# Optimization experiments

Hardware: AMD Instinct MI355X
Metric: run time of the kernel (lower is better)

Reference implementation:

```python
import jax, jax.numpy as jnp
import numpy as np

B, T, D, H, K, M = 2, 2048, 1024, 16, 3, 16384
HD = D // H
SCALE = D * (H ** 0.5)  # faithful to source: n_embd / n_head**(-0.5)


def _normalize(v, axis=-1, eps=1e-12):
    # torch F.normalize: v / max(||v||, eps)
    n = jnp.sqrt(jnp.sum(v * v, axis=axis, keepdims=True))
    return v / jnp.maximum(n, eps)


def setup_inputs() -> dict:
    key = jax.random.key(0)
    ks = jax.random.split(key, 12)
    s = 1.0 / np.sqrt(D)
    return {
        "x": jax.random.normal(ks[0], (B, T, D), jnp.float32),
        "Wq": jax.random.normal(ks[1], (D, D), jnp.float32) * s,
        "bq": jax.random.normal(ks[2], (D,), jnp.float32) * 0.01,
        "Wk": jax.random.normal(ks[3], (D, D), jnp.float32) * s,
        "bk": jax.random.normal(ks[4], (D,), jnp.float32) * 0.01,
        "Wv": jax.random.normal(ks[5], (D, D), jnp.float32) * s,
        "bv": jax.random.normal(ks[6], (D,), jnp.float32) * 0.01,
        "Wo": jax.random.normal(ks[7], (D, D), jnp.float32) * s,
        "bo": jax.random.normal(ks[8], (D,), jnp.float32) * 0.01,
        "gate_bias": jax.random.normal(ks[9], (H, 1, 1), jnp.float32),
        "mem_bank": jax.random.normal(ks[10], (B, M, 2, D), jnp.float32) * s,
        "knn_idx": jax.random.randint(ks[11], (B, T, K), 0, M, jnp.int32),
    }


def reference(x, Wq, bq, Wk, bk, Wv, bv, Wo, bo, gate_bias, mem_bank, knn_idx):
    b, t, d = x.shape
    # projections + L2-normalize q,k (as in source)
    q = _normalize(x @ Wq.T + bq)
    k = _normalize(x @ Wk.T + bk)
    v = x @ Wv.T + bv
    # split heads: b t (h hd) -> b h t hd
    q = q.reshape(b, t, H, HD).transpose(0, 2, 1, 3)
    k = k.reshape(b, t, H, HD).transpose(0, 2, 1, 3)
    v = v.reshape(b, t, H, HD).transpose(0, 2, 1, 3)
    # local causal attention (hand-rolled, dropout is eval no-op)
    qk = jnp.einsum('bhid,bhjd->bhij', q, k) * SCALE  # [b,h,t,t]
    causal = jnp.triu(jnp.ones((t, t), dtype=bool), 1)
    qk = jnp.where(causal, -jnp.inf, qk)
    attn = jax.nn.softmax(qk, axis=-1)
    qkv = jnp.einsum('bhij,bhjd->bhid', attn, v)  # [b,h,t,hd]
    # kNN memory retrieval: gather top-k (key,value) memories per token
    mem = mem_bank[jnp.arange(b)[:, None, None], knn_idx]  # [b,t,k,2,D]
    mem_k = mem[..., 0, :].reshape(b, t, K, H, HD).transpose(0, 3, 1, 2, 4)  # [b,h,t,k,hd]
    mem_v = mem[..., 1, :].reshape(b, t, K, H, HD).transpose(0, 3, 1, 2, 4)
    mem_qk = jnp.einsum('bhtd,bhtkd->bhtk', q.astype(jnp.float32), mem_k) * SCALE
    mem_attn = jax.nn.softmax(mem_qk, axis=-1)
    mem_qkv = jnp.einsum('bhtk,bhtkd->bhtd', mem_attn, mem_v)
    # per-head gated blend, bf16 round-trip (source casts to bfloat16)
    combined = mem_qkv * gate_bias + qkv * (1.0 - gate_bias)  # gate [H,1,1] broadcasts
    combined = combined.astype(jnp.bfloat16).astype(jnp.float32)
    y = combined.transpose(0, 2, 1, 3).reshape(b, t, d)  # b h t hd -> b t D
    return y @ Wo.T + bo
```

## Files before the change

### kernel.cpp

```cpp
#include <hip/hip_runtime.h>
#include <math.h>

#define B_ 2
#define T_ 2048
#define D_ 1024
#define H_ 16
#define HD_ 64
#define M_ 16384
#define SCALE_F 4096.0f
#define LDP 3072
#define ST 72

using short8 = __attribute__((ext_vector_type(8))) short;
using bf16x8 = __attribute__((ext_vector_type(8))) __bf16;
using f32x4  = __attribute__((ext_vector_type(4))) float;

__device__ __forceinline__ unsigned short f2bf(float x){
  unsigned u = __builtin_bit_cast(unsigned, x);
  u += 0x7fffu + ((u >> 16) & 1u);
  return (unsigned short)(u >> 16);
}
__device__ __forceinline__ float bf2f(unsigned short h){
  unsigned u = ((unsigned)h) << 16;
  return __builtin_bit_cast(float, u);
}

__device__ __forceinline__ float wsum(float v){
  #pragma unroll
  for (int off = 32; off; off >>= 1) v += __shfl_xor(v, off);
  return v;
}

__device__ __forceinline__ void ld_g2l16(const unsigned short* g, unsigned short* l){
  __builtin_amdgcn_global_load_lds(
      (const __attribute__((address_space(1))) void*)g,
      (__attribute__((address_space(3))) void*)l, 16, 0, 0);
}

__global__ __launch_bounds__(256)
void cvt_all(const float* __restrict__ x, const float* __restrict__ Wq,
             const float* __restrict__ Wk, const float* __restrict__ Wv,
             const float* __restrict__ Wo,
             unsigned short* __restrict__ Xhi, unsigned short* __restrict__ Xlo,
             unsigned short* __restrict__ Whi, unsigned short* __restrict__ Wlo,
             unsigned short* __restrict__ Wohi)
{
  const int i = blockIdx.x*256 + threadIdx.x;
  const float* src; unsigned short* hi; unsigned short* lo = nullptr; int rel;
  if      (i < 1048576){ src = x;  hi = Xhi;            lo = Xlo;            rel = i; }
  else if (i < 1310720){ src = Wq; hi = Whi;            lo = Wlo;            rel = i - 1048576; }
  else if (i < 1572864){ src = Wk; hi = Whi + 1048576;  lo = Wlo + 1048576;  rel = i - 1310720; }
  else if (i < 1835008){ src = Wv; hi = Whi + 2097152;                       rel = i - 1572864; }
  else                 { src = Wo; hi = Wohi;                                rel = i - 1835008; }
  float4 v = *(const float4*)(src + (size_t)rel*4);
  unsigned short h0=f2bf(v.x), h1=f2bf(v.y), h2=f2bf(v.z), h3=f2bf(v.w);
  uint2 hh; hh.x = (unsigned)h0 | ((unsigned)h1 << 16);
            hh.y = (unsigned)h2 | ((unsigned)h3 << 16);
  *(uint2*)(hi + (size_t)rel*4) = hh;
  if (lo){
    uint2 ll;
    ll.x = (unsigned)f2bf(v.x-bf2f(h0)) | ((unsigned)f2bf(v.y-bf2f(h1)) << 16);
    ll.y = (unsigned)f2bf(v.z-bf2f(h2)) | ((unsigned)f2bf(v.w-bf2f(h3)) << 16);
    *(uint2*)(lo + (size_t)rel*4) = ll;
  }
}

template<bool COMP>
__global__ __launch_bounds__(256)
void gemm_lds(const unsigned short* __restrict__ Ahi_g, const unsigned short* __restrict__ Alo_g,
              const unsigned short* __restrict__ Bhi_g, const unsigned short* __restrict__ Blo_g,
              const float* __restrict__ bias0, const float* __restrict__ bias1,
              const float* __restrict__ bias2,
              float* __restrict__ C, int ldc)
{
  __shared__ __align__(16) unsigned short Ah[128*32];
  __shared__ __align__(16) unsigned short Bh[128*32];
  __shared__ __align__(16) unsigned short Al[COMP ? 128*32 : 8];
  __shared__ __align__(16) unsigned short Bl[COMP ? 128*32 : 8];

  const int tid = threadIdx.x, lane = tid & 63, wv = tid >> 6;
  const int wm = wv >> 1, wn = wv & 1;
  const int mi = lane & 15, quad = lane >> 4;

  int bid = blockIdx.y*gridDim.x + blockIdx.x;
  const int cpx = (gridDim.x*gridDim.y) >> 3;
  bid = (bid & 7)*cpx + (bid >> 3);
  const int n0 = (bid % gridDim.x) * 128;
  const int m0 = (bid / gridDim.x) * 128;

  const int seg = n0 >> 10;
  const float* bias = (seg == 0) ? bias0 : (seg == 1) ? bias1 : bias2;
  const int nw = n0 & 1023;
  const bool comp = COMP && (seg < 2);

  f32x4 acc[4][4];
  #pragma unroll
  for (int a = 0; a < 4; ++a)
    #pragma unroll
    for (int b = 0; b < 4; ++b)
      acc[a][b] = (f32x4){0.f, 0.f, 0.f, 0.f};

  for (int k0 = 0; k0 < 1024; k0 += 32){
    __syncthreads();
    #pragma unroll
    for (int t = 0; t < 2; ++t){
      int j = wv*128 + t*64 + lane;
      int row = j >> 2, c16 = j & 3;
      size_t ga = (size_t)(m0 + row)*1024 + k0 + c16*8;
      size_t gb = (size_t)(n0 + row)*1024 + k0 + c16*8;
      ld_g2l16(Ahi_g + ga, Ah + j*8);
      ld_g2l16(Bhi_g + gb, Bh + j*8);
      if (comp){
        ld_g2l16(Alo_g + ga, Al + j*8);
        ld_g2l16(Blo_g + gb, Bl + j*8);
      }
    }
    __syncthreads();

    bf16x8 ah[4], al[4];
    #pragma unroll
    for (int a = 0; a < 4; ++a){
      int r = wm*64 + a*16 + mi;
      ah[a] = __builtin_bit_cast(bf16x8, *(const short8*)(Ah + r*32 + quad*8));
      if (comp)
        al[a] = __builtin_bit_cast(bf16x8, *(const short8*)(Al + r*32 + quad*8));
    }
    #pragma unroll
    for (int b = 0; b < 4; ++b){
      int r = wn*64 + b*16 + mi;
      bf16x8 bh = __builtin_bit_cast(bf16x8, *(const short8*)(Bh + r*32 + quad*8));
      if (comp){
        bf16x8 bl = __builtin_bit_cast(bf16x8, *(const short8*)(Bl + r*32 + quad*8));
        #pragma unroll
        for (int a = 0; a < 4; ++a){
          acc[a][b] = __builtin_amdgcn_mfma_f32_16x16x32_bf16(al[a], bh, acc[a][b], 0, 0, 0);
          acc[a][b] = __builtin_amdgcn_mfma_f32_16x16x32_bf16(ah[a], bl, acc[a][b], 0, 0, 0);
          acc[a][b] = __builtin_amdgcn_mfma_f32_16x16x32_bf16(ah[a], bh, acc[a][b], 0, 0, 0);
        }
      } else {
        #pragma unroll
        for (int a = 0; a < 4; ++a)
          acc[a][b] = __builtin_amdgcn_mfma_f32_16x16x32_bf16(ah[a], bh, acc[a][b], 0, 0, 0);
      }
    }
  }
  #pragma unroll
  for (int a = 0; a < 4; ++a)
    #pragma unroll
    for (int b = 0; b < 4; ++b)
      #pragma unroll
      for (int r = 0; r < 4; ++r){
        int row  = m0 + wm*64 + a*16 + quad*4 + r;
        int coll = wn*64 + b*16 + mi;
        C[(size_t)row*ldc + n0 + coll] = acc[a][b][r] + bias[nw + coll];
      }
}

__global__ __launch_bounds__(256)
void norm_split(const float* __restrict__ P,
                unsigned short* __restrict__ Qhi, unsigned short* __restrict__ Qlo,
                unsigned short* __restrict__ Khi, unsigned short* __restrict__ Klo,
                unsigned short* __restrict__ Vbf)
{
  const int row = blockIdx.x, tid = threadIdx.x;
  const int bb = row >> 11, t = row & 2047;
  const int lane = tid & 63, wv = tid >> 6;
  const size_t base = (size_t)row * LDP;
  float4 q4 = *(const float4*)(P + base + tid*4);
  float4 k4 = *(const float4*)(P + base + 1024 + tid*4);
  float4 v4 = *(const float4*)(P + base + 2048 + tid*4);
  float sq = wsum(q4.x*q4.x + q4.y*q4.y + q4.z*q4.z + q4.w*q4.w);
  float sk = wsum(k4.x*k4.x + k4.y*k4.y + k4.z*k4.z + k4.w*k4.w);
  __shared__ float rq[4], rk[4];
  if (lane == 0){ rq[wv] = sq; rk[wv] = sk; }
  __syncthreads();
  float cq = 1.f / fmaxf(sqrtf(rq[0]+rq[1]+rq[2]+rq[3]), 1e-12f);
  float ck = 1.f / fmaxf(sqrtf(rk[0]+rk[1]+rk[2]+rk[3]), 1e-12f);
  float qf[4] = {q4.x*cq, q4.y*cq, q4.z*cq, q4.w*cq};
  float kf[4] = {k4.x*ck, k4.y*ck, k4.z*ck, k4.w*ck};

  const int h = tid >> 4, d0 = (tid & 15)*4;
  const size_t ob = ((size_t)(bb*H_ + h)*T_ + t)*64 + d0;

  uint2 qh, ql, kh, kl, vv;
  unsigned short t0,t1,t2,t3;
  t0=f2bf(qf[0]); t1=f2bf(qf[1]); t2=f2bf(qf[2]); t3=f2bf(qf[3]);
  qh.x = t0 | ((unsigned)t1<<16); qh.y = t2 | ((unsigned)t3<<16);
  ql.x = f2bf(qf[0]-bf2f(t0)) | ((unsigned)f2bf(qf[1]-bf2f(t1))<<16);
  ql.y = f2bf(qf[2]-bf2f(t2)) | ((unsigned)f2bf(qf[3]-bf2f(t3))<<16);
  t0=f2bf(kf[0]); t1=f2bf(kf[1]); t2=f2bf(kf[2]); t3=f2bf(kf[3]);
  kh.x = t0 | ((unsigned)t1<<16); kh.y = t2 | ((unsigned)t3<<16);
  kl.x = f2bf(kf[0]-bf2f(t0)) | ((unsigned)f2bf(kf[1]-bf2f(t1))<<16);
  kl.y = f2bf(kf[2]-bf2f(t2)) | ((unsigned)f2bf(kf[3]-bf2f(t3))<<16);
  vv.x = f2bf(v4.x) | ((unsigned)f2bf(v4.y)<<16);
  vv.y = f2bf(v4.z) | ((unsigned)f2bf(v4.w)<<16);
  *(uint2*)(Qhi + ob) = qh;  *(uint2*)(Qlo + ob) = ql;
  *(uint2*)(Khi + ob) = kh;  *(uint2*)(Klo + ob) = kl;
  *(uint2*)(Vbf + ob) = vv;
}

__device__ __forceinline__ void stage_issue(
    const unsigned short* __restrict__ Khi_g, const unsigned short* __restrict__ Klo_g,
    const unsigned short* __restrict__ Vbf, size_t hb, int jt, int tid,
    uint2* khr, uint2* klr, ushort4* vra, ushort4* vrb)
{
  #pragma unroll
  for (int i = 0; i < 4; ++i){
    int idx = tid + i*256;
    int row = idx >> 4, c4 = idx & 15;
    size_t g = (hb + jt*64 + row)*64 + c4*4;
    khr[i] = *(const uint2*)(Khi_g + g);
    klr[i] = *(const uint2*)(Klo_g + g);
  }
  #pragma unroll
  for (int i = 0; i < 2; ++i){
    int idx = tid + i*256;
    int rp = idx & 31, d4 = idx >> 5;
    size_t g = (hb + jt*64 + 2*rp)*64 + d4*4;
    vra[i] = *(const ushort4*)(Vbf + g);
    vrb[i] = *(const ushort4*)(Vbf + g + 64);
  }
}

__device__ __forceinline__ void stage_write(char* bufc, int tid,
    const uint2* khr, const uint2* klr, const ushort4* vra, const ushort4* vrb)
{
  unsigned short* Kh = (unsigned short*)bufc;
  unsigned short* Kl = (unsigned short*)(bufc + 9216);
  unsigned* vt = (unsigned*)(bufc + 18432);
  #pragma unroll
  for (int i = 0; i < 4; ++i){
    int idx = tid + i*256;
    int row = idx >> 4, c4 = idx & 15;
    *(uint2*)(Kh + row*ST + c4*4) = khr[i];
    *(uint2*)(Kl + row*ST + c4*4) = klr[i];
  }
  #pragma unroll
  for (int i = 0; i < 2; ++i){
    int idx = tid + i*256;
    int rp = idx & 31, d4 = idx >> 5;
    vt[(d4*4+0)*36 + rp] = (unsigned)vra[i].x | ((unsigned)vrb[i].x << 16);
    vt[(d4*4+1)*36 + rp] = (unsigned)vra[i].y | ((unsigned)vrb[i].y << 16);
    vt[(d4*4+2)*36 + rp] = (unsigned)vra[i].z | ((unsigned)vrb[i].z << 16);
    vt[(d4*4+3)*36 + rp] = (unsigned)vra[i].w | ((unsigned)vrb[i].w << 16);
  }
}

__device__ __forceinline__ void attn_tile(
    const unsigned short* __restrict__ Kh, const unsigned short* __restrict__ Kl,
    const unsigned short* __restrict__ Vt, unsigned short* __restrict__ pw,
    const bf16x8* qh, const bf16x8* ql,
    f32x4* O, float& mr, float& lr,
    bool last, int relrow, int mi, int quad)
{
  f32x4 st[4];
  #pragma unroll
  for (int mt = 0; mt < 4; ++mt) st[mt] = (f32x4){0.f,0.f,0.f,0.f};
  __builtin_amdgcn_s_setprio(1);
  #pragma unroll
  for (int mt = 0; mt < 4; ++mt){
    int krow = mt*16 + mi;
    #pragma unroll
    for (int ks = 0; ks < 2; ++ks){
      bf16x8 kh = __builtin_bit_cast(bf16x8, *(const short8*)(Kh + krow*ST + ks*32 + quad*8));
      bf16x8 kl = __builtin_bit_cast(bf16x8, *(const short8*)(Kl + krow*ST + ks*32 + quad*8));
      st[mt] = __builtin_amdgcn_mfma_f32_16x16x32_bf16(kl, qh[ks], st[mt], 0, 0, 0);
      st[mt] = __builtin_amdgcn_mfma_f32_16x16x32_bf16(kh, ql[ks], st[mt], 0, 0, 0);
      st[mt] = __builtin_amdgcn_mfma_f32_16x16x32_bf16(kh, qh[ks], st[mt], 0, 0, 0);
    }
  }
  __builtin_amdgcn_s_setprio(0);

  float tmax = -INFINITY;
  #pragma unroll
  for (int mt = 0; mt < 4; ++mt)
    #pragma unroll
    for (int r = 0; r < 4; ++r){
      float s = st[mt][r] * SCALE_F;
      if (last){
        int key = mt*16 + quad*4 + r;
        if (key > relrow) s = -INFINITY;
      }
      st[mt][r] = s;
      tmax = fmaxf(tmax, s);
    }
  tmax = fmaxf(tmax, __shfl_xor(tmax, 16));
  tmax = fmaxf(tmax, __shfl_xor(tmax, 32));
  float mnew = fmaxf(mr, tmax);
  float alpha = __expf(mr - mnew);
  mr = mnew;
  float tsum = 0.f;
  #pragma unroll
  for (int mt = 0; mt < 4; ++mt)
    #pragma unroll
    for (int r = 0; r < 4; ++r){
      float p = __expf(st[mt][r] - mnew);
      st[mt][r] = p;
      tsum += p;
    }
  tsum += __shfl_xor(tsum, 16);
  tsum += __shfl_xor(tsum, 32);
  lr = lr*alpha + tsum;

  #pragma unroll
  for (int mt = 0; mt < 4; ++mt){
    uint2 pk;
    pk.x = (unsigned)f2bf(st[mt][0]) | ((unsigned)f2bf(st[mt][1]) << 16);
    pk.y = (unsigned)f2bf(st[mt][2]) | ((unsigned)f2bf(st[mt][3]) << 16);
    *(uint2*)(pw + mi*ST + mt*16 + quad*4) = pk;
  }

  float af[4];
  #pragma unroll
  for (int r = 0; r < 4; ++r) af[r] = __shfl(alpha, quad*4 + r);
  #pragma unroll
  for (int dn = 0; dn < 4; ++dn)
    #pragma unroll
    for (int r = 0; r < 4; ++r) O[dn][r] *= af[r];

  __builtin_amdgcn_s_setprio(1);
  #pragma unroll
  for (int kt = 0; kt < 2; ++kt){
    bf16x8 pf = __builtin_bit_cast(bf16x8, *(const short8*)(pw + mi*ST + kt*32 + quad*8));
    #pragma unroll
    for (int dn = 0; dn < 4; ++dn){
      bf16x8 vf = __builtin_bit_cast(bf16x8, *(const short8*)(Vt + (dn*16 + mi)*ST + kt*32 + quad*8));
      O[dn] = __builtin_amdgcn_mfma_f32_16x16x32_bf16(pf, vf, O[dn], 0, 0, 0);
    }
  }
  __builtin_amdgcn_s_setprio(0);
}

__global__ __launch_bounds__(256)
void attn_knn(const unsigned short* __restrict__ Qhi, const unsigned short* __restrict__ Qlo,
              const unsigned short* __restrict__ Khi_g, const unsigned short* __restrict__ Klo_g,
              const unsigned short* __restrict__ Vbf,
              const float* __restrict__ mem_bank, const int* __restrict__ knn_idx,
              const float* __restrict__ gate_bias, unsigned short* __restrict__ comb)
{
  __shared__ __align__(16) char smpool[64512];
  float* qkvs = (float*)smpool;

  const int bb = blockIdx.z, h = blockIdx.y;
  const int p = blockIdx.x;
  const int jA = p, jB = 31 - p;
  const int tid = threadIdx.x, lane = tid & 63, wv = tid >> 6;
  const int mi = lane & 15, quad = lane >> 4;
  const int relrow = wv*16 + mi;
  const size_t hb = (size_t)(bb*H_ + h)*T_;
  unsigned short* pw = (unsigned short*)(smpool + 55296) + wv*1152;

  const int sub = lane & 3;
  const int grp = tid >> 2;
  const int base = lane & 60;
  int idxP[2];
  idxP[0] = (sub < 3) ? knn_idx[((size_t)bb*T_ + jA*64 + grp)*3 + sub] : 0;
  idxP[1] = (sub < 3) ? knn_idx[((size_t)bb*T_ + jB*64 + grp)*3 + sub] : 0;

  bf16x8 qhA[2], qlA[2], qhB[2], qlB[2];
  #pragma unroll
  for (int ks = 0; ks < 2; ++ks){
    qhA[ks] = __builtin_bit_cast(bf16x8, *(const uint4*)(Qhi + (hb + jA*64 + relrow)*64 + ks*32 + quad*8));
    qlA[ks] = __builtin_bit_cast(bf16x8, *(const uint4*)(Qlo + (hb + jA*64 + relrow)*64 + ks*32 + quad*8));
    qhB[ks] = __builtin_bit_cast(bf16x8, *(const uint4*)(Qhi + (hb + jB*64 + relrow)*64 + ks*32 + quad*8));
    qlB[ks] = __builtin_bit_cast(bf16x8, *(const uint4*)(Qlo + (hb + jB*64 + relrow)*64 + ks*32 + quad*8));
  }

  f32x4 OA[4], OB[4];
  #pragma unroll
  for (int dn = 0; dn < 4; ++dn){
    OA[dn] = (f32x4){0.f,0.f,0.f,0.f};
    OB[dn] = (f32x4){0.f,0.f,0.f,0.f};
  }
  float mA = -INFINITY, lA = 0.f, mB = -INFINITY, lB = 0.f;

  const int ntiles = jB + 1;

  uint2 khr[4], klr[4]; ushort4 vra[2], vrb[2];
  stage_issue(Khi_g, Klo_g, Vbf, hb, 0, tid, khr, klr, vra, vrb);
  stage_write(smpool, tid, khr, klr, vra, vrb);
  stage_issue(Khi_g, Klo_g, Vbf, hb, 1, tid, khr, klr, vra, vrb);

  int cur = 0;
  for (int jt = 0; jt < ntiles; ++jt){
    __syncthreads();
    if (jt + 1 < ntiles){
      stage_write(smpool + (cur^1)*27648, tid, khr, klr, vra, vrb);
      if (jt + 2 < ntiles)
        stage_issue(Khi_g, Klo_g, Vbf, hb, jt+2, tid, khr, klr, vra, vrb);
    }
    char* bufc = smpool + cur*27648;
    const unsigned short* Kh = (const unsigned short*)bufc;
    const unsigned short* Kl = (const unsigned short*)(bufc + 9216);
    const unsigned short* Vt = (const unsigned short*)(bufc + 18432);
    if (jt <= jA)
      attn_tile(Kh, Kl, Vt, pw, qhA, qlA, OA, mA, lA, jt == jA, relrow, mi, quad);
    attn_tile(Kh, Kl, Vt, pw, qhB, qlB, OB, mB, lB, jt == jB, relrow, mi, quad);
    cur ^= 1;
  }

  __syncthreads();
  {
    float liA[4], liB[4];
    #pragma unroll
    for (int r = 0; r < 4; ++r){
      liA[r] = 1.f / __shfl(lA, quad*4 + r);
      liB[r] = 1.f / __shfl(lB, quad*4 + r);
    }
    #pragma unroll
    for (int dn = 0; dn < 4; ++dn)
      #pragma unroll
      for (int r = 0; r < 4; ++r){
        qkvs[(      wv*16 + quad*4 + r)*68 + dn*16 + mi] = OA[dn][r] * liA[r];
        qkvs[(64 +  wv*16 + quad*4 + r)*68 + dn*16 + mi] = OB[dn][r] * liB[r];
      }
  }
  __syncthreads();

  const float g = gate_bias[h];
  const float gq = 1.f - g;

  #pragma unroll
  for (int it = 0; it < 2; ++it){
    const int jq = it ? jB : jA;
    const int trow = jq*64 + grp;
    const int lrow = it*64 + grp;

    int idxs[3];
    #pragma unroll
    for (int kk = 0; kk < 3; ++kk) idxs[kk] = __shfl(idxP[it], base + kk);

    float4 mk4[3][4], mv4[3][4];
    #pragma unroll
    for (int kk = 0; kk < 3; ++kk){
      const float* mk = mem_bank + (((size_t)bb*M_ + idxs[kk])*2 + 0)*D_ + h*HD_ + sub*16;
      const float* mv = mem_bank + (((size_t)bb*M_ + idxs[kk])*2 + 1)*D_ + h*HD_ + sub*16;
      #pragma unroll
      for (int j4 = 0; j4 < 4; ++j4){
        mk4[kk][j4] = *(const float4*)(mk + j4*4);
        mv4[kk][j4] = *(const float4*)(mv + j4*4);
      }
    }

    float qf[16];
    {
      const unsigned short* qp = Qhi + (hb + trow)*64 + sub*16;
      const unsigned short* lp = Qlo + (hb + trow)*64 + sub*16;
      unsigned short hs[16], ls[16];
      *(uint4*)hs     = *(const uint4*)qp;
      *(uint4*)(hs+8) = *(const uint4*)(qp+8);
      *(uint4*)ls     = *(const uint4*)lp;
      *(uint4*)(ls+8) = *(const uint4*)(lp+8);
      #pragma unroll
      for (int j = 0; j < 16; ++j) qf[j] = bf2f(hs[j]) + bf2f(ls[j]);
    }

    float dts[3]; float mx = -INFINITY;
    #pragma unroll
    for (int kk = 0; kk < 3; ++kk){
      float dsum = 0.f;
      #pragma unroll
      for (int j4 = 0; j4 < 4; ++j4){
        float4 m4 = mk4[kk][j4];
        dsum += qf[j4*4+0]*m4.x + qf[j4*4+1]*m4.y + qf[j4*4+2]*m4.z + qf[j4*4+3]*m4.w;
      }
      dsum += __shfl_xor(dsum, 1);
      dsum += __shfl_xor(dsum, 2);
      dsum *= SCALE_F;
      dts[kk] = dsum;
      mx = fmaxf(mx, dsum);
    }
    float e0 = __expf(dts[0]-mx), e1 = __expf(dts[1]-mx), e2 = __expf(dts[2]-mx);
    float inv = 1.f/(e0+e1+e2);
    float w[3] = {e0*inv, e1*inv, e2*inv};

    float ov[16];
    #pragma unroll
    for (int j = 0; j < 16; ++j) ov[j] = 0.f;
    #pragma unroll
    for (int kk = 0; kk < 3; ++kk){
      #pragma unroll
      for (int j4 = 0; j4 < 4; ++j4){
        float4 m4 = mv4[kk][j4];
        ov[j4*4+0] += w[kk]*m4.x;
        ov[j4*4+1] += w[kk]*m4.y;
        ov[j4*4+2] += w[kk]*m4.z;
        ov[j4*4+3] += w[kk]*m4.w;
      }
    }

    unsigned short os[16];
    #pragma unroll
    for (int j = 0; j < 16; ++j){
      float qkv = qkvs[lrow*68 + sub*16 + j];
      os[j] = f2bf(ov[j]*g + qkv*gq);
    }
    unsigned short* op = comb + ((size_t)bb*T_ + trow)*D_ + h*HD_ + sub*16;
    *(uint4*)op     = *(uint4*)os;
    *(uint4*)(op+8) = *(uint4*)(os+8);
  }
}

extern "C" void kernel_launch(void* const* d_in, const int* in_sizes, int n_in,
                              void* d_out, int out_size, void* d_ws, size_t ws_size,
                              hipStream_t stream)
{
  (void)in_sizes; (void)n_in; (void)out_size; (void)ws_size;
  const float* x    = (const float*)d_in[0];
  const float* Wq   = (const float*)d_in[1];
  const float* bq   = (const float*)d_in[2];
  const float* Wk   = (const float*)d_in[3];
  const float* bk   = (const float*)d_in[4];
  const float* Wv   = (const float*)d_in[5];
  const float* bv   = (const float*)d_in[6];
  const float* Wo   = (const float*)d_in[7];
  const float* bo   = (const float*)d_in[8];
  const float* gate = (const float*)d_in[9];
  const float* mem  = (const float*)d_in[10];
  const int*   knn  = (const int*)d_in[11];

  char* ws = (char*)d_ws;
  float*          P    = (float*)ws;
  unsigned short* comb = (unsigned short*)ws;
  unsigned short* Qhi  = (unsigned short*)(ws +  50331648);
  unsigned short* Qlo  = (unsigned short*)(ws +  58720256);
  unsigned short* Khi  = (unsigned short*)(ws +  67108864);
  unsigned short* Klo  = (unsigned short*)(ws +  75497472);
  unsigned short* Vbf  = (unsigned short*)(ws +  83886080);
  unsigned short* Xhi  = (unsigned short*)(ws +  92274688);
  unsigned short* Xlo  = (unsigned short*)(ws + 100663296);
  unsigned short* Whi  = (unsigned short*)(ws + 109051904);
  unsigned short* Wlo  = (unsigned short*)(ws + 115343360);
  unsigned short* Wohi = (unsigned short*)(ws + 119537664);

  cvt_all<<<8192, 256, 0, stream>>>(x, Wq, Wk, Wv, Wo, Xhi, Xlo, Whi, Wlo, Wohi);
  gemm_lds<true><<<dim3(24, 32), 256, 0, stream>>>(Xhi, Xlo, Whi, Wlo, bq, bk, bv, P, LDP);
  norm_split<<<4096, 256, 0, stream>>>(P, Qhi, Qlo, Khi, Klo, Vbf);
  attn_knn<<<dim3(T_/128, H_, B_), 256, 0, stream>>>(Qhi, Qlo, Khi, Klo, Vbf,
                                                     mem, knn, gate, comb);
  gemm_lds<false><<<dim3(8, 32), 256, 0, stream>>>(comb, nullptr, Wohi, nullptr,
                                                   bo, bo, bo, (float*)d_out, D_);
}
```

Measured before the change: 562.0 us.

## Fuse V bf16 head-major write into QKV GEMM epilogue and remap attention grid per XCD

```diff
diff --git a/kernel.cpp b/kernel.cpp
--- a/kernel.cpp
+++ b/kernel.cpp
@@ -71,7 +71,8 @@
               const unsigned short* __restrict__ Bhi_g, const unsigned short* __restrict__ Blo_g,
               const float* __restrict__ bias0, const float* __restrict__ bias1,
               const float* __restrict__ bias2,
-              float* __restrict__ C, int ldc)
+              float* __restrict__ C, int ldc,
+              unsigned short* __restrict__ Vout)
 {
   __shared__ __align__(16) unsigned short Ah[128*32];
   __shared__ __align__(16) unsigned short Bh[128*32];
@@ -144,23 +145,38 @@
       }
     }
   }
-  #pragma unroll
-  for (int a = 0; a < 4; ++a)
-    #pragma unroll
-    for (int b = 0; b < 4; ++b)
-      #pragma unroll
-      for (int r = 0; r < 4; ++r){
-        int row  = m0 + wm*64 + a*16 + quad*4 + r;
-        int coll = wn*64 + b*16 + mi;
-        C[(size_t)row*ldc + n0 + coll] = acc[a][b][r] + bias[nw + coll];
-      }
+
+  if (COMP && seg == 2){
+    #pragma unroll
+    for (int a = 0; a < 4; ++a)
+      #pragma unroll
+      for (int b = 0; b < 4; ++b)
+        #pragma unroll
+        for (int r = 0; r < 4; ++r){
+          int row = m0 + wm*64 + a*16 + quad*4 + r;
+          int col = nw + wn*64 + b*16 + mi;
+          int bb2 = row >> 11, t2 = row & 2047;
+          Vout[(((size_t)(bb2*H_ + (col >> 6))*T_ + t2) << 6) + (col & 63)] =
+              f2bf(acc[a][b][r] + bias[col]);
+        }
+  } else {
+    #pragma unroll
+    for (int a = 0; a < 4; ++a)
+      #pragma unroll
+      for (int b = 0; b < 4; ++b)
+        #pragma unroll
+        for (int r = 0; r < 4; ++r){
+          int row  = m0 + wm*64 + a*16 + quad*4 + r;
+          int coll = wn*64 + b*16 + mi;
+          C[(size_t)row*ldc + n0 + coll] = acc[a][b][r] + bias[nw + coll];
+        }
+  }
 }
 
 __global__ __launch_bounds__(256)
 void norm_split(const float* __restrict__ P,
                 unsigned short* __restrict__ Qhi, unsigned short* __restrict__ Qlo,
-                unsigned short* __restrict__ Khi, unsigned short* __restrict__ Klo,
-                unsigned short* __restrict__ Vbf)
+                unsigned short* __restrict__ Khi, unsigned short* __restrict__ Klo)
 {
   const int row = blockIdx.x, tid = threadIdx.x;
   const int bb = row >> 11, t = row & 2047;
@@ -168,7 +184,6 @@
   const size_t base = (size_t)row * LDP;
   float4 q4 = *(const float4*)(P + base + tid*4);
   float4 k4 = *(const float4*)(P + base + 1024 + tid*4);
-  float4 v4 = *(const float4*)(P + base + 2048 + tid*4);
   float sq = wsum(q4.x*q4.x + q4.y*q4.y + q4.z*q4.z + q4.w*q4.w);
   float sk = wsum(k4.x*k4.x + k4.y*k4.y + k4.z*k4.z + k4.w*k4.w);
   __shared__ float rq[4], rk[4];
@@ -182,7 +197,7 @@
   const int h = tid >> 4, d0 = (tid & 15)*4;
   const size_t ob = ((size_t)(bb*H_ + h)*T_ + t)*64 + d0;
 
-  uint2 qh, ql, kh, kl, vv;
+  uint2 qh, ql, kh, kl;
   unsigned short t0,t1,t2,t3;
   t0=f2bf(qf[0]); t1=f2bf(qf[1]); t2=f2bf(qf[2]); t3=f2bf(qf[3]);
   qh.x = t0 | ((unsigned)t1<<16); qh.y = t2 | ((unsigned)t3<<16);
@@ -192,11 +207,8 @@
   kh.x = t0 | ((unsigned)t1<<16); kh.y = t2 | ((unsigned)t3<<16);
   kl.x = f2bf(kf[0]-bf2f(t0)) | ((unsigned)f2bf(kf[1]-bf2f(t1))<<16);
   kl.y = f2bf(kf[2]-bf2f(t2)) | ((unsigned)f2bf(kf[3]-bf2f(t3))<<16);
-  vv.x = f2bf(v4.x) | ((unsigned)f2bf(v4.y)<<16);
-  vv.y = f2bf(v4.z) | ((unsigned)f2bf(v4.w)<<16);
   *(uint2*)(Qhi + ob) = qh;  *(uint2*)(Qlo + ob) = ql;
   *(uint2*)(Khi + ob) = kh;  *(uint2*)(Klo + ob) = kl;
-  *(uint2*)(Vbf + ob) = vv;
 }
 
 __device__ __forceinline__ void stage_issue(
@@ -341,8 +353,11 @@
   __shared__ __align__(16) char smpool[64512];
   float* qkvs = (float*)smpool;
 
-  const int bb = blockIdx.z, h = blockIdx.y;
-  const int p = blockIdx.x;
+  const int id = blockIdx.x;
+  const int xcd = id & 7, slot = id >> 3;
+  const int g_ = (slot >> 4)*8 + xcd;
+  const int bb = g_ >> 4, h = g_ & 15;
+  const int p = slot & 15;
   const int jA = p, jB = 31 - p;
   const int tid = threadIdx.x, lane = tid & 63, wv = tid >> 6;
   const int mi = lane & 15, quad = lane >> 4;
@@ -534,10 +549,9 @@
   unsigned short* Wohi = (unsigned short*)(ws + 119537664);
 
   cvt_all<<<8192, 256, 0, stream>>>(x, Wq, Wk, Wv, Wo, Xhi, Xlo, Whi, Wlo, Wohi);
-  gemm_lds<true><<<dim3(24, 32), 256, 0, stream>>>(Xhi, Xlo, Whi, Wlo, bq, bk, bv, P, LDP);
-  norm_split<<<4096, 256, 0, stream>>>(P, Qhi, Qlo, Khi, Klo, Vbf);
-  attn_knn<<<dim3(T_/128, H_, B_), 256, 0, stream>>>(Qhi, Qlo, Khi, Klo, Vbf,
-                                                     mem, knn, gate, comb);
+  gemm_lds<true><<<dim3(24, 32), 256, 0, stream>>>(Xhi, Xlo, Whi, Wlo, bq, bk, bv, P, LDP, Vbf);
+  norm_split<<<4096, 256, 0, stream>>>(P, Qhi, Qlo, Khi, Klo);
+  attn_knn<<<512, 256, 0, stream>>>(Qhi, Qlo, Khi, Klo, Vbf, mem, knn, gate, comb);
   gemm_lds<false><<<dim3(8, 32), 256, 0, stream>>>(comb, nullptr, Wohi, nullptr,
-                                                   bo, bo, bo, (float*)d_out, D_);
-}
+                                                   bo, bo, bo, (float*)d_out, D_, nullptr);
+}
```

Result: no change. 554.9 us (-1.3%).
